# Optimization experiments

Measured on AMD Instinct MI355X. Metric: run time of the kernel, lower is better.

Reference implementation:

```python
import jax, jax.numpy as jnp
import numpy as np

HDIM = 32
U_DIM = 8
HID = 128
T = 65536
DYN_GAIN = 0.02
STATE_DAMP = 0.1
H_CLIP = 5.0
DT = np.float32(5.0 / 60.0)  # 5 minutes in hours


def _xavier(key, shape):
    fan_in, fan_out = shape[0], shape[1]
    limit = np.sqrt(6.0 / (fan_in + fan_out)).astype(np.float32)
    return jax.random.uniform(key, shape, jnp.float32, -limit, limit)


def setup_inputs() -> dict:
    key = jax.random.key(0)
    ks = jax.random.split(key, 8)
    U = jax.random.normal(ks[0], (T, U_DIM), jnp.float32)
    params = {
        "U": U,
        "h0": jnp.zeros((1, HDIM), jnp.float32),
        "W1": _xavier(ks[1], (HDIM + U_DIM, HID)), "b1": jnp.zeros((HID,), jnp.float32),
        "W2": _xavier(ks[2], (HID, HID)), "b2": jnp.zeros((HID,), jnp.float32),
        "W3": _xavier(ks[3], (HID, HDIM)), "b3": jnp.zeros((HDIM,), jnp.float32),
        "Wd": _xavier(ks[4], (HDIM, 1)), "bd": jnp.zeros((1,), jnp.float32),
        "Wt": _xavier(ks[5], (HDIM, 1)), "bt": jnp.zeros((1,), jnp.float32),
        "Wc": _xavier(ks[6], (HDIM, 1)), "bc": jnp.zeros((1,), jnp.float32),
    }
    return params


def reference(U, h0, W1, b1, W2, b2, W3, b3, Wd, bd, Wt, bt, Wc, bc):
    dt = jnp.float32(DT)

    def dyn(h, u):
        # h: [1, HDIM], u: [1, U_DIM]
        x = jnp.concatenate([h, u], axis=-1)
        z = jax.nn.silu(x @ W1 + b1)
        z = jax.nn.silu(z @ W2 + b2)
        drift = z @ W3 + b3
        return DYN_GAIN * drift - STATE_DAMP * h

    def step(h, u_t):
        u = u_t[None, :]  # [1, U_DIM]
        # readout of current state (before the RK4 step, as in the torch loop)
        d = (h @ Wd + bd)[..., 0]  # [1]
        t = (h @ Wt + bt)[..., 0]
        c = (h @ Wc + bc)[..., 0]
        k1 = dyn(h, u)
        k2 = dyn(h + 0.5 * dt * k1, u)
        k3 = dyn(h + 0.5 * dt * k2, u)
        k4 = dyn(h + dt * k3, u)
        h_next = h + dt / 6.0 * (k1 + 2.0 * k2 + 2.0 * k3 + k4)
        h_next = jnp.nan_to_num(h_next, nan=0.0, posinf=0.0, neginf=0.0)
        h_next = jnp.clip(jnp.tanh(h_next), -H_CLIP, H_CLIP)
        return h_next, (d, t, c)

    h_last, (ds, ts, cs) = jax.lax.scan(step, h0, U)
    # ds/ts/cs: [T, 1] -> [T]
    return ds.squeeze(-1), ts.squeeze(-1), cs.squeeze(-1), h_last
```

## Files before the change

kernel.cpp:

```cpp
#include <hip/hip_runtime.h>
#include <math.h>


constexpr int T_STEPS = 65536;
constexpr int HD  = 32;
constexpr int HID = 128;

typedef float v2f __attribute__((ext_vector_type(2)));

__device__ __forceinline__ v2f fma2(v2f a, v2f b, v2f c) {
    return __builtin_elementwise_fma(a, b, c);
}

__device__ __forceinline__ float silu_f(float a) {
    return a / (1.0f + __expf(-a));
}

__device__ __forceinline__ void wg_barrier() {
    asm volatile("s_waitcnt lgkmcnt(0)" ::: "memory");
    __builtin_amdgcn_s_barrier();
    asm volatile("" ::: "memory");
}

__global__ __launch_bounds__(256, 1)
void node_scan(const float* __restrict__ U,
               const float* __restrict__ h0,
               const float* __restrict__ W1, const float* __restrict__ b1,
               const float* __restrict__ W2, const float* __restrict__ b2,
               const float* __restrict__ W3, const float* __restrict__ b3,
               const float* __restrict__ Wd, const float* __restrict__ bd,
               const float* __restrict__ Wt, const float* __restrict__ bt,
               const float* __restrict__ Wc, const float* __restrict__ bc,
               float* __restrict__ out)
{
    const int tid = threadIdx.x;
    const int lam = tid & 63;
    const int w   = tid >> 6;
    const int wk  = w & 1;
    const int wo  = w >> 1;
    const int j1  = lam + wk * 64;
    const int o   = lam + wo * 64;
    const int m   = tid & 31;
    const int sub = (tid >> 5) & 1;

    __shared__ __align__(16) float xbuf[HD];
    __shared__ __align__(16) float z1buf[HID];
    __shared__ __align__(16) float z2buf[HID];
    __shared__ __align__(16) float pex[2 * HID];
    __shared__ __align__(16) float pdrift[64];

    v2f w1p[20];
#pragma unroll
    for (int i = 0; i < 20; ++i) {
        w1p[i].x = W1[(2 * i) * HID + j1];
        w1p[i].y = W1[(2 * i + 1) * HID + j1];
    }
    const float b1r = b1[j1];

    v2f w2p[32];
#pragma unroll
    for (int kp = 0; kp < 32; ++kp) {
        const int k = wk * 64 + 2 * kp;
        w2p[kp].x = W2[k * HID + o];
        w2p[kp].y = W2[(k + 1) * HID + o];
    }
    const float b2r = b2[o];

    v2f w3p[16];
#pragma unroll
    for (int i = 0; i < 16; ++i) {
        const int u0 = wo * 64 + sub * 32 + 2 * i;
        w3p[i].x = W3[u0 * HD + m];
        w3p[i].y = W3[(u0 + 1) * HD + m];
    }
    const float b3r = b3[m];

    const float whr = (w == 0) ? Wd[m] : (w == 1) ? Wt[m] : (w == 2) ? Wc[m] : 0.0f;
    const float bh  = (w == 0) ? bd[0] : (w == 1) ? bt[0] : (w == 2) ? bc[0] : 0.0f;

    float hm   = h0[m];
    float xm   = hm;
    float kacc = 0.0f;

    const float DT  = 5.0f / 60.0f;
    const float HDT = 0.5f * DT;
    const float W6  = DT / 6.0f;

    float4 ua = *(const float4*)(U);
    float4 ub = *(const float4*)(U + 4);

    xbuf[m] = xm;
    wg_barrier();

    for (int t = 0; t < T_STEPS; ++t) {
        const int tn = (t + 1 < T_STEPS) ? (t + 1) : t;
        const float4 na = *(const float4*)(U + tn * 8);
        const float4 nb = *(const float4*)(U + tn * 8 + 4);

        {
            float p = hm * whr;
            p += __shfl_xor(p, 16);
            p += __shfl_xor(p, 8);
            p += __shfl_xor(p, 4);
            p += __shfl_xor(p, 2);
            p += __shfl_xor(p, 1);
            if (lam == 0 && w < 3) out[w * T_STEPS + t] = p + bh;
        }

        float upj;
        {
            v2f u0; u0.x = ua.x; u0.y = ua.y;
            v2f u1; u1.x = ua.z; u1.y = ua.w;
            v2f u2; u2.x = ub.x; u2.y = ub.y;
            v2f u3; u3.x = ub.z; u3.y = ub.w;
            v2f up = {b1r, 0.0f};
            up = fma2(u0, w1p[16], up);
            up = fma2(u1, w1p[17], up);
            up = fma2(u2, w1p[18], up);
            up = fma2(u3, w1p[19], up);
            upj = up.x + up.y;
        }

#pragma unroll
        for (int st = 0; st < 4; ++st) {
            v2f a0 = {upj, 0.0f}, a1 = {0.0f, 0.0f};
            const float4* xv = (const float4*)xbuf;
#pragma unroll
            for (int i4 = 0; i4 < 8; ++i4) {
                const float4 v = xv[i4];
                v2f lo; lo.x = v.x; lo.y = v.y;
                v2f hi; hi.x = v.z; hi.y = v.w;
                a0 = fma2(lo, w1p[2 * i4],     a0);
                a1 = fma2(hi, w1p[2 * i4 + 1], a1);
            }
            const v2f as = a0 + a1;
            z1buf[j1] = silu_f(as.x + as.y);
            __builtin_amdgcn_wave_barrier();

            v2f c0 = {0.0f, 0.0f}, c1 = {0.0f, 0.0f};
            const float4* z1v = (const float4*)(z1buf + wk * 64);
#pragma unroll
            for (int i4 = 0; i4 < 16; ++i4) {
                const float4 v = z1v[i4];
                v2f lo; lo.x = v.x; lo.y = v.y;
                v2f hi; hi.x = v.z; hi.y = v.w;
                c0 = fma2(lo, w2p[2 * i4],     c0);
                c1 = fma2(hi, w2p[2 * i4 + 1], c1);
            }
            const v2f cs = c0 + c1;
            const float mine = cs.x + cs.y;
            pex[wk * HID + o] = mine;
            wg_barrier();

            const float po = pex[(1 ^ wk) * HID + o];
            const float z2 = silu_f(mine + po + b2r);
            z2buf[o] = z2;
            __builtin_amdgcn_wave_barrier();

            v2f p0 = {0.0f, 0.0f}, p1 = {0.0f, 0.0f};
            const float4* z2v = (const float4*)(z2buf + wo * 64 + sub * 32);
#pragma unroll
            for (int i4 = 0; i4 < 8; ++i4) {
                const float4 v = z2v[i4];
                v2f lo; lo.x = v.x; lo.y = v.y;
                v2f hi; hi.x = v.z; hi.y = v.w;
                p0 = fma2(lo, w3p[2 * i4],     p0);
                p1 = fma2(hi, w3p[2 * i4 + 1], p1);
            }
            const v2f ps = p0 + p1;
            float pr = ps.x + ps.y;
            pr += __shfl_xor(pr, 32);
            pdrift[wo * 32 + m] = pr;
            wg_barrier();

            {
                const float drift = (pdrift[m] + pdrift[m + 32]) + b3r;
                const float k = 0.02f * drift - 0.1f * xm;
                if (st == 0)      { kacc = k;           xm = hm + HDT * k; }
                else if (st == 1) { kacc += 2.0f * k;   xm = hm + HDT * k; }
                else if (st == 2) { kacc += 2.0f * k;   xm = hm + DT  * k; }
                else {
                    kacc += k;
                    float hn = hm + W6 * kacc;
                    if (!isfinite(hn)) hn = 0.0f;
                    hn = tanhf(hn);
                    hn = fminf(fmaxf(hn, -5.0f), 5.0f);
                    hm = hn; xm = hn;
                }
                xbuf[m] = xm;
            }
            __builtin_amdgcn_wave_barrier();
        }
        ua = na; ub = nb;
    }

    if (tid < HD) out[3 * T_STEPS + tid] = hm;
}

extern "C" void kernel_launch(void* const* d_in, const int* in_sizes, int n_in,
                              void* d_out, int out_size, void* d_ws, size_t ws_size,
                              hipStream_t stream) {
    const float* U  = (const float*)d_in[0];
    const float* h0 = (const float*)d_in[1];
    const float* W1 = (const float*)d_in[2];
    const float* b1 = (const float*)d_in[3];
    const float* W2 = (const float*)d_in[4];
    const float* b2 = (const float*)d_in[5];
    const float* W3 = (const float*)d_in[6];
    const float* b3 = (const float*)d_in[7];
    const float* Wd = (const float*)d_in[8];
    const float* bd = (const float*)d_in[9];
    const float* Wt = (const float*)d_in[10];
    const float* bt = (const float*)d_in[11];
    const float* Wc = (const float*)d_in[12];
    const float* bc = (const float*)d_in[13];
    float* out = (float*)d_out;

    node_scan<<<1, 256, 0, stream>>>(U, h0, W1, b1, W2, b2, W3, b3,
                                     Wd, bd, Wt, bt, Wc, bc, out);
}
```

Baseline: 221.9 ms.

## Compute layer-3 drift redundantly per wave to drop LDS reduction round trip

Each wave now computes all 128 second-layer activations and the full third-layer matvec itself, combining the two 64-wide halves with a cross-lane shuffle instead of writing partials to shared memory and re-reading them after a barrier. The second-layer partial sums are stored interleaved as float2 so each lane can fetch both halves in one read. This aims to shorten the serial per-stage critical path, which is dominated by LDS traffic and synchronisation, at the cost of duplicated silu and FMA work and more registers per thread.

Result: slower. 244.7 ms (+10.3%).

```diff
diff --git a/kernel.cpp b/kernel.cpp
--- a/kernel.cpp
+++ b/kernel.cpp
@@ -40,14 +40,13 @@
     const int wo  = w >> 1;
     const int j1  = lam + wk * 64;
     const int o   = lam + wo * 64;
-    const int m   = tid & 31;
-    const int sub = (tid >> 5) & 1;
-
-    __shared__ __align__(16) float xbuf[HD];
-    __shared__ __align__(16) float z1buf[HID];
-    __shared__ __align__(16) float z2buf[HID];
-    __shared__ __align__(16) float pex[2 * HID];
-    __shared__ __align__(16) float pdrift[64];
+    const int m   = lam & 31;
+    const int sub = lam >> 5;
+
+    __shared__ __align__(16) float  xbuf[HD];
+    __shared__ __align__(16) float  z1buf[HID];
+    __shared__ __align__(16) float  z2buf[HID];
+    __shared__ __align__(16) float2 pex2[HID];
 
     v2f w1p[20];
 #pragma unroll
@@ -64,12 +63,12 @@
         w2p[kp].x = W2[k * HID + o];
         w2p[kp].y = W2[(k + 1) * HID + o];
     }
-    const float b2r = b2[o];
-
-    v2f w3p[16];
-#pragma unroll
-    for (int i = 0; i < 16; ++i) {
-        const int u0 = wo * 64 + sub * 32 + 2 * i;
+    const float b2a = b2[lam], b2b = b2[lam + 64];
+
+    v2f w3p[32];
+#pragma unroll
+    for (int i = 0; i < 32; ++i) {
+        const int u0 = sub * 64 + 2 * i;
         w3p[i].x = W3[u0 * HD + m];
         w3p[i].y = W3[(u0 + 1) * HD + m];
     }
@@ -149,46 +148,52 @@
             }
             const v2f cs = c0 + c1;
             const float mine = cs.x + cs.y;
-            pex[wk * HID + o] = mine;
+            ((float*)&pex2[o])[wk] = mine;
             wg_barrier();
 
-            const float po = pex[(1 ^ wk) * HID + o];
-            const float z2 = silu_f(mine + po + b2r);
-            z2buf[o] = z2;
+            const float2 e0 = pex2[lam];
+            const float2 e1 = pex2[lam + 64];
+            const float z2A = silu_f(e0.x + e0.y + b2a);
+            const float z2B = silu_f(e1.x + e1.y + b2b);
+            z2buf[lam]      = z2A;
+            z2buf[lam + 64] = z2B;
             __builtin_amdgcn_wave_barrier();
 
             v2f p0 = {0.0f, 0.0f}, p1 = {0.0f, 0.0f};
-            const float4* z2v = (const float4*)(z2buf + wo * 64 + sub * 32);
-#pragma unroll
-            for (int i4 = 0; i4 < 8; ++i4) {
+            v2f p2 = {0.0f, 0.0f}, p3 = {0.0f, 0.0f};
+            const float4* z2v = (const float4*)(z2buf + sub * 64);
+#pragma unroll
+            for (int i4 = 0; i4 < 16; ++i4) {
                 const float4 v = z2v[i4];
                 v2f lo; lo.x = v.x; lo.y = v.y;
                 v2f hi; hi.x = v.z; hi.y = v.w;
-                p0 = fma2(lo, w3p[2 * i4],     p0);
-                p1 = fma2(hi, w3p[2 * i4 + 1], p1);
-            }
-            const v2f ps = p0 + p1;
+                if (i4 & 1) {
+                    p2 = fma2(lo, w3p[2 * i4],     p2);
+                    p3 = fma2(hi, w3p[2 * i4 + 1], p3);
+                } else {
+                    p0 = fma2(lo, w3p[2 * i4],     p0);
+                    p1 = fma2(hi, w3p[2 * i4 + 1], p1);
+                }
+            }
+            const v2f ps = (p0 + p1) + (p2 + p3);
             float pr = ps.x + ps.y;
             pr += __shfl_xor(pr, 32);
-            pdrift[wo * 32 + m] = pr;
+            const float drift = pr + b3r;
             wg_barrier();
 
-            {
-                const float drift = (pdrift[m] + pdrift[m + 32]) + b3r;
-                const float k = 0.02f * drift - 0.1f * xm;
-                if (st == 0)      { kacc = k;           xm = hm + HDT * k; }
-                else if (st == 1) { kacc += 2.0f * k;   xm = hm + HDT * k; }
-                else if (st == 2) { kacc += 2.0f * k;   xm = hm + DT  * k; }
-                else {
-                    kacc += k;
-                    float hn = hm + W6 * kacc;
-                    if (!isfinite(hn)) hn = 0.0f;
-                    hn = tanhf(hn);
-                    hn = fminf(fmaxf(hn, -5.0f), 5.0f);
-                    hm = hn; xm = hn;
-                }
-                xbuf[m] = xm;
-            }
+            const float k = 0.02f * drift - 0.1f * xm;
+            if (st == 0)      { kacc = k;           xm = hm + HDT * k; }
+            else if (st == 1) { kacc += 2.0f * k;   xm = hm + HDT * k; }
+            else if (st == 2) { kacc += 2.0f * k;   xm = hm + DT  * k; }
+            else {
+                kacc += k;
+                float hn = hm + W6 * kacc;
+                if (!isfinite(hn)) hn = 0.0f;
+                hn = tanhf(hn);
+                hn = fminf(fmaxf(hn, -5.0f), 5.0f);
+                hm = hn; xm = hn;
+            }
+            xbuf[m] = xm;
             __builtin_amdgcn_wave_barrier();
         }
         ua = na; ub = nb;
```
